# Kernel tuning notes

Hardware: AMD Instinct MI355X
Metric: run time of the kernel (lower is better)

## Reference

```python
import jax, jax.numpy as jnp
import numpy as np
from math import sqrt

N, D = 8192, 64

def setup_inputs() -> dict:
    key = jax.random.key(0)
    kq, kk, kv = jax.random.split(key, 3)
    q = jax.random.normal(kq, (N, D), dtype=jnp.float32)
    k = jax.random.normal(kk, (N, D), dtype=jnp.float32)
    v = jax.random.normal(kv, (N, D), dtype=jnp.float32)
    return {"q": q, "k": k, "v": v}

def reference(q, k, v):
    # Mathematically identical to the block-wise online-softmax loop:
    # after processing all KV blocks, m_blk == rowmax(S), l_blk == rowsum(exp(S - m)),
    # O = (exp(S - m) @ V) / l.
    scale = 1.0 / sqrt(q.shape[-1])
    S = (q @ k.T) * scale            # [N, N] attention scores
    m = jnp.max(S, axis=1, keepdims=True)   # running max -> global row max
    P = jnp.exp(S - m)                      # unnormalized probs
    L = jnp.sum(P, axis=1, keepdims=True)   # softmax denominator, [N, 1]
    O = (P @ v) / L                          # [N, D]
    return (O, L)
```

## Files before the change

### kernel.cpp

```cpp
#include <hip/hip_runtime.h>
#include <hip/hip_bf16.h>
#include <math.h>

#define N 8192
#define D 64
#define QSCALE 0.18033688011112042f

typedef __attribute__((ext_vector_type(8))) short short8;
typedef __attribute__((ext_vector_type(16))) float f32x16;
typedef __attribute__((ext_vector_type(4))) unsigned int ui4;

__device__ inline short f32_to_bf16_bits(float x) {
    unsigned u = __builtin_bit_cast(unsigned, x);
    u += 0x7FFFu + ((u >> 16) & 1u);
    return (short)(u >> 16);
}
__device__ inline float bfbits_to_f32(unsigned short u) {
    return __builtin_bit_cast(float, ((unsigned)u) << 16);
}
__device__ inline unsigned cvt_pk_bf16(float a, float b) {
    unsigned r;
    asm("v_cvt_pk_bf16_f32 %0, %1, %2" : "=v"(r) : "v"(a), "v"(b));
    return r;
}
__device__ inline float max3f(float a, float b, float c) {
    float d;
    asm("v_max3_f32 %0, %1, %2, %3" : "=v"(d) : "v"(a), "v"(b), "v"(c));
    return d;
}

__global__ __launch_bounds__(256) void fa_conv(const float* __restrict__ q,
                                               const float* __restrict__ k,
                                               const float* __restrict__ v,
                                               short* __restrict__ Qb,
                                               short* __restrict__ Kp,
                                               short* __restrict__ Vp) {
    int bid = blockIdx.x, tid = threadIdx.x;
    if (bid < 512) {
        int i = (bid * 256 + tid) * 4;
        float4 a = *(const float4*)(q + i);
        unsigned lo = cvt_pk_bf16(a.x * QSCALE, a.y * QSCALE);
        unsigned hi = cvt_pk_bf16(a.z * QSCALE, a.w * QSCALE);
        unsigned long long u = (unsigned long long)lo | ((unsigned long long)hi << 32);
        *(unsigned long long*)(Qb + i) = u;
    } else if (bid < 768) {
        int t = bid - 512;
        int c = tid >> 6, l = tid & 63, ql = l & 31, hi = l >> 5;
        const float* src = k + (size_t)(t * 32 + ql) * D + c * 16 + hi * 8;
        float4 a = *(const float4*)(src);
        float4 b = *(const float4*)(src + 4);
        uint4 u = { cvt_pk_bf16(a.x, a.y), cvt_pk_bf16(a.z, a.w),
                    cvt_pk_bf16(b.x, b.y), cvt_pk_bf16(b.z, b.w) };
        *(uint4*)(Kp + (size_t)t * 2048 + c * 512 + l * 8) = u;
    } else {
        int t = bid - 768;
        int dt = tid >> 7, h = (tid >> 6) & 1, hi = (tid >> 5) & 1, ql = tid & 31;
        const float* src = v + (size_t)(t * 32 + h * 16 + hi * 4) * D + dt * 32 + ql;
        float f[8];
#pragma unroll
        for (int j = 0; j < 8; ++j)
            f[j] = src[(size_t)((j & 3) + 8 * (j >> 2)) * D];
        uint4 u = { cvt_pk_bf16(f[0], f[1]), cvt_pk_bf16(f[2], f[3]),
                    cvt_pk_bf16(f[4], f[5]), cvt_pk_bf16(f[6], f[7]) };
        *(uint4*)(Vp + (size_t)t * 2048 + dt * 1024 + h * 512 + hi * 256 + ql * 8) = u;
    }
}

__global__ __launch_bounds__(256) void fa_part_kernel(const short* __restrict__ Qb,
                                                      const short* __restrict__ Kp,
                                                      const short* __restrict__ Vp,
                                                      short* __restrict__ OTb,
                                                      float* __restrict__ Ml,
                                                      int KN) {
    const int qt = blockIdx.x & 63;
    const int s  = blockIdx.x >> 6;
    const int w = threadIdx.x >> 6, lane = threadIdx.x & 63;
    const int ql = lane & 31, hi = lane >> 5;
    const int qrow = qt * 128 + w * 32 + ql;

    const short* qp = Qb + (size_t)qrow * D + hi * 8;
    short8 qf0 = *(const short8*)(qp);
    short8 qf1 = *(const short8*)(qp + 16);
    short8 qf2 = *(const short8*)(qp + 32);
    short8 qf3 = *(const short8*)(qp + 48);

    f32x16 acc0 = {}, acc1 = {};
    float mex = -INFINITY, lsum = 0.f;

    const int t0 = (s * KN) >> 5, nt = KN >> 5;
    const short* kp = Kp + (size_t)t0 * 2048 + lane * 8;
    const short* vp = Vp + (size_t)t0 * 2048 + lane * 8;

    short8 kA0, kA1, kA2, kA3, kB0, kB1, kB2, kB3;
    short8 vf0, vf1, vf2, vf3;

#define LOADK(d0, d1, d2, d3) do {                                         \
        d0 = *(const short8*)(kp);                                         \
        d1 = *(const short8*)(kp + 512);                                   \
        d2 = *(const short8*)(kp + 1024);                                  \
        d3 = *(const short8*)(kp + 1536);                                  \
        kp += 2048;                                                        \
    } while (0)
#define LOADV() do {                                                       \
        vf0 = *(const short8*)(vp);                                        \
        vf1 = *(const short8*)(vp + 512);                                  \
        vf2 = *(const short8*)(vp + 1024);                                 \
        vf3 = *(const short8*)(vp + 1536);                                 \
        vp += 2048;                                                        \
    } while (0)

#define TILE(K0, K1, K2, K3) do {                                           \
        __builtin_amdgcn_s_setprio(1);                                      \
        f32x16 st = {};                                                     \
        st = __builtin_amdgcn_mfma_f32_32x32x16_bf16(K0, qf0, st, 0, 0, 0); \
        st = __builtin_amdgcn_mfma_f32_32x32x16_bf16(K1, qf1, st, 0, 0, 0); \
        st = __builtin_amdgcn_mfma_f32_32x32x16_bf16(K2, qf2, st, 0, 0, 0); \
        st = __builtin_amdgcn_mfma_f32_32x32x16_bf16(K3, qf3, st, 0, 0, 0); \
        __builtin_amdgcn_s_setprio(0);                                      \
        float m0_ = max3f(st[0], st[1], st[2]);                             \
        float m1_ = max3f(st[3], st[4], st[5]);                             \
        float m2_ = max3f(st[6], st[7], st[8]);                             \
        float m3_ = max3f(st[9], st[10], st[11]);                           \
        float m4_ = max3f(st[12], st[13], st[14]);                          \
        mex = max3f(mex, max3f(m0_, m1_, m2_), max3f(m3_, m4_, st[15]));    \
        unsigned pk0, pk1, pk2, pk3, pk4, pk5, pk6, pk7;                    \
        float rs_;                                                          \
        {                                                                   \
            float a_, b_;                                                   \
            a_ = __builtin_amdgcn_exp2f(st[0]);  b_ = __builtin_amdgcn_exp2f(st[1]);  \
            rs_ = a_ + b_;         pk0 = cvt_pk_bf16(a_, b_);               \
            a_ = __builtin_amdgcn_exp2f(st[2]);  b_ = __builtin_amdgcn_exp2f(st[3]);  \
            rs_ += a_ + b_;        pk1 = cvt_pk_bf16(a_, b_);               \
            a_ = __builtin_amdgcn_exp2f(st[4]);  b_ = __builtin_amdgcn_exp2f(st[5]);  \
            rs_ += a_ + b_;        pk2 = cvt_pk_bf16(a_, b_);               \
            a_ = __builtin_amdgcn_exp2f(st[6]);  b_ = __builtin_amdgcn_exp2f(st[7]);  \
            rs_ += a_ + b_;        pk3 = cvt_pk_bf16(a_, b_);               \
            a_ = __builtin_amdgcn_exp2f(st[8]);  b_ = __builtin_amdgcn_exp2f(st[9]);  \
            rs_ += a_ + b_;        pk4 = cvt_pk_bf16(a_, b_);               \
            a_ = __builtin_amdgcn_exp2f(st[10]); b_ = __builtin_amdgcn_exp2f(st[11]); \
            rs_ += a_ + b_;        pk5 = cvt_pk_bf16(a_, b_);               \
            a_ = __builtin_amdgcn_exp2f(st[12]); b_ = __builtin_amdgcn_exp2f(st[13]); \
            rs_ += a_ + b_;        pk6 = cvt_pk_bf16(a_, b_);               \
            a_ = __builtin_amdgcn_exp2f(st[14]); b_ = __builtin_amdgcn_exp2f(st[15]); \
            rs_ += a_ + b_;        pk7 = cvt_pk_bf16(a_, b_);               \
        }                                                                   \
        lsum += rs_;                                                        \
        ui4 va_ = { pk0, pk1, pk2, pk3 };                                   \
        ui4 vb_ = { pk4, pk5, pk6, pk7 };                                   \
        short8 pb0 = __builtin_bit_cast(short8, va_);                       \
        short8 pb1 = __builtin_bit_cast(short8, vb_);                       \
        __builtin_amdgcn_s_setprio(1);                                      \
        acc0 = __builtin_amdgcn_mfma_f32_32x32x16_bf16(vf0, pb0, acc0, 0, 0, 0); \
        acc0 = __builtin_amdgcn_mfma_f32_32x32x16_bf16(vf1, pb1, acc0, 0, 0, 0); \
        acc1 = __builtin_amdgcn_mfma_f32_32x32x16_bf16(vf2, pb0, acc1, 0, 0, 0); \
        acc1 = __builtin_amdgcn_mfma_f32_32x32x16_bf16(vf3, pb1, acc1, 0, 0, 0); \
        __builtin_amdgcn_s_setprio(0);                                      \
    } while (0)

    LOADK(kA0, kA1, kA2, kA3);
#pragma unroll 1
    for (int T = 0; T < nt; T += 2) {
        LOADV();
        LOADK(kB0, kB1, kB2, kB3);
        TILE(kA0, kA1, kA2, kA3);
        LOADV();
        if (T + 2 < nt) LOADK(kA0, kA1, kA2, kA3);
        TILE(kB0, kB1, kB2, kB3);
    }
#undef LOADK
#undef LOADV
#undef TILE

    mex = fmaxf(mex, __shfl_xor(mex, 32));
    lsum += __shfl_xor(lsum, 32);

#pragma unroll
    for (int r = 0; r < 16; ++r) {
        int d0 = (r & 3) + 8 * (r >> 2) + 4 * hi;
        OTb[(size_t)(s * 64 + d0) * N + qrow]      = f32_to_bf16_bits(acc0[r]);
        OTb[(size_t)(s * 64 + 32 + d0) * N + qrow] = f32_to_bf16_bits(acc1[r]);
    }
    if (hi == 0) {
        Ml[(size_t)(s * 2 + 0) * N + qrow] = lsum;
        Ml[(size_t)(s * 2 + 1) * N + qrow] = mex;
    }
}

__global__ __launch_bounds__(256) void fa_comb_kernel(const short* __restrict__ OTb,
                                                      const float* __restrict__ Ml,
                                                      float* __restrict__ Out, int S) {
    const int qb = blockIdx.x >> 2, db4 = blockIdx.x & 3;
    const int row = threadIdx.x & 63, dd = threadIdx.x >> 6;
    const int grow = qb * 64 + row;
    const int d0 = db4 * 16 + dd * 4;

    float v0 = 0.f, v1 = 0.f, v2 = 0.f, v3 = 0.f;
    float L = 0.f, mg = -INFINITY;
    for (int s = 0; s < S; ++s) {
        size_t base = (size_t)(s * 64 + d0) * N + grow;
        v0 += bfbits_to_f32((unsigned short)OTb[base]);
        v1 += bfbits_to_f32((unsigned short)OTb[base + (size_t)N]);
        v2 += bfbits_to_f32((unsigned short)OTb[base + (size_t)2 * N]);
        v3 += bfbits_to_f32((unsigned short)OTb[base + (size_t)3 * N]);
        L  += Ml[(size_t)(s * 2 + 0) * N + grow];
        mg = fmaxf(mg, Ml[(size_t)(s * 2 + 1) * N + grow]);
    }
    float inv = 1.0f / L;
    float4 o = { v0 * inv, v1 * inv, v2 * inv, v3 * inv };
    *(float4*)(Out + (size_t)grow * D + d0) = o;
    if (db4 == 0 && dd == 0) Out[(size_t)N * D + grow] = exp2f(-mg) * L;
}

extern "C" void kernel_launch(void* const* d_in, const int* in_sizes, int n_in,
                              void* d_out, int out_size, void* d_ws, size_t ws_size,
                              hipStream_t stream) {
    const float* q = (const float*)d_in[0];
    const float* k = (const float*)d_in[1];
    const float* v = (const float*)d_in[2];
    float* out = (float*)d_out;

    short* Qb = (short*)d_ws;
    short* Kp = Qb + (size_t)N * D;
    short* Vp = Kp + (size_t)N * D;
    short* OTb = (short*)((char*)d_ws + 3 * 1048576);

    int S = 16;
    while (S > 1 &&
           3ull * 1048576 + (size_t)S * (64ull * N * 2) + (size_t)S * (2ull * N * 4) > ws_size)
        S >>= 1;
    float* Ml = (float*)(OTb + (size_t)S * 64 * N);
    int KN = N / S;

    fa_conv<<<1024, 256, 0, stream>>>(q, k, v, Qb, Kp, Vp);
    fa_part_kernel<<<64 * S, 256, 0, stream>>>(Qb, Kp, Vp, OTb, Ml, KN);
    fa_comb_kernel<<<(N / 64) * 4, 256, 0, stream>>>(OTb, Ml, out, S);
}
```

Measured before the change: 45.30 us.

## Double-buffer V fragments, reorder block mapping, drop setprio hints

```diff
diff --git a/kernel.cpp b/kernel.cpp
--- a/kernel.cpp
+++ b/kernel.cpp
@@ -72,8 +72,8 @@
                                                       short* __restrict__ OTb,
                                                       float* __restrict__ Ml,
                                                       int KN) {
-    const int qt = blockIdx.x & 63;
-    const int s  = blockIdx.x >> 6;
+    const int s  = blockIdx.x & 15;
+    const int qt = blockIdx.x >> 4;
     const int w = threadIdx.x >> 6, lane = threadIdx.x & 63;
     const int ql = lane & 31, hi = lane >> 5;
     const int qrow = qt * 128 + w * 32 + ql;
@@ -92,7 +92,7 @@
     const short* vp = Vp + (size_t)t0 * 2048 + lane * 8;
 
     short8 kA0, kA1, kA2, kA3, kB0, kB1, kB2, kB3;
-    short8 vf0, vf1, vf2, vf3;
+    short8 vA0, vA1, vA2, vA3, vB0, vB1, vB2, vB3;
 
 #define LOADK(d0, d1, d2, d3) do {                                         \
         d0 = *(const short8*)(kp);                                         \
@@ -101,22 +101,20 @@
         d3 = *(const short8*)(kp + 1536);                                  \
         kp += 2048;                                                        \
     } while (0)
-#define LOADV() do {                                                       \
-        vf0 = *(const short8*)(vp);                                        \
-        vf1 = *(const short8*)(vp + 512);                                  \
-        vf2 = *(const short8*)(vp + 1024);                                 \
-        vf3 = *(const short8*)(vp + 1536);                                 \
+#define LOADV(d0, d1, d2, d3) do {                                         \
+        d0 = *(const short8*)(vp);                                         \
+        d1 = *(const short8*)(vp + 512);                                   \
+        d2 = *(const short8*)(vp + 1024);                                  \
+        d3 = *(const short8*)(vp + 1536);                                  \
         vp += 2048;                                                        \
     } while (0)
 
-#define TILE(K0, K1, K2, K3) do {                                           \
-        __builtin_amdgcn_s_setprio(1);                                      \
+#define TILE(K0, K1, K2, K3, V0, V1, V2, V3) do {                           \
         f32x16 st = {};                                                     \
         st = __builtin_amdgcn_mfma_f32_32x32x16_bf16(K0, qf0, st, 0, 0, 0); \
         st = __builtin_amdgcn_mfma_f32_32x32x16_bf16(K1, qf1, st, 0, 0, 0); \
         st = __builtin_amdgcn_mfma_f32_32x32x16_bf16(K2, qf2, st, 0, 0, 0); \
         st = __builtin_amdgcn_mfma_f32_32x32x16_bf16(K3, qf3, st, 0, 0, 0); \
-        __builtin_amdgcn_s_setprio(0);                                      \
         float m0_ = max3f(st[0], st[1], st[2]);                             \
         float m1_ = max3f(st[3], st[4], st[5]);                             \
         float m2_ = max3f(st[6], st[7], st[8]);                             \
@@ -149,23 +147,24 @@
         ui4 vb_ = { pk4, pk5, pk6, pk7 };                                   \
         short8 pb0 = __builtin_bit_cast(short8, va_);                       \
         short8 pb1 = __builtin_bit_cast(short8, vb_);                       \
-        __builtin_amdgcn_s_setprio(1);                                      \
-        acc0 = __builtin_amdgcn_mfma_f32_32x32x16_bf16(vf0, pb0, acc0, 0, 0, 0); \
-        acc0 = __builtin_amdgcn_mfma_f32_32x32x16_bf16(vf1, pb1, acc0, 0, 0, 0); \
-        acc1 = __builtin_amdgcn_mfma_f32_32x32x16_bf16(vf2, pb0, acc1, 0, 0, 0); \
-        acc1 = __builtin_amdgcn_mfma_f32_32x32x16_bf16(vf3, pb1, acc1, 0, 0, 0); \
-        __builtin_amdgcn_s_setprio(0);                                      \
+        acc0 = __builtin_amdgcn_mfma_f32_32x32x16_bf16(V0, pb0, acc0, 0, 0, 0); \
+        acc0 = __builtin_amdgcn_mfma_f32_32x32x16_bf16(V1, pb1, acc0, 0, 0, 0); \
+        acc1 = __builtin_amdgcn_mfma_f32_32x32x16_bf16(V2, pb0, acc1, 0, 0, 0); \
+        acc1 = __builtin_amdgcn_mfma_f32_32x32x16_bf16(V3, pb1, acc1, 0, 0, 0); \
     } while (0)
 
     LOADK(kA0, kA1, kA2, kA3);
+    LOADV(vA0, vA1, vA2, vA3);
 #pragma unroll 1
     for (int T = 0; T < nt; T += 2) {
-        LOADV();
         LOADK(kB0, kB1, kB2, kB3);
-        TILE(kA0, kA1, kA2, kA3);
-        LOADV();
-        if (T + 2 < nt) LOADK(kA0, kA1, kA2, kA3);
-        TILE(kB0, kB1, kB2, kB3);
+        LOADV(vB0, vB1, vB2, vB3);
+        TILE(kA0, kA1, kA2, kA3, vA0, vA1, vA2, vA3);
+        if (T + 2 < nt) {
+            LOADK(kA0, kA1, kA2, kA3);
+            LOADV(vA0, vA1, vA2, vA3);
+        }
+        TILE(kB0, kB1, kB2, kB3, vB0, vB1, vB2, vB3);
     }
 #undef LOADK
 #undef LOADV
```

After: 45.36 us. No clear change (+0.1%).
